# Kernel tuning notes

Measured on AMD Instinct MI355X. Metric: run time of the kernel, lower is better.

The kernel has to match this reference:

```python
import jax, jax.numpy as jnp
import numpy as np


def _diffuse(x, A):
    # x: [B,C,N,L], A: [B,V,W] -> out[b,c,v,l] = sum_w x[b,c,w,l] * A[b,v,w]
    return jnp.einsum('ncwl,nvw->ncvl', x, A)


def setup_inputs() -> dict:
    key = jax.random.key(0)
    kx, k0, k1, k2, kw = jax.random.split(key, 5)
    B, C, N, L = 32, 40, 512, 12
    C_OUT = 20
    C_CAT = 7 * C  # (order*support_len + 1) * c_in = (2*3+1)*40
    x = jax.random.normal(kx, (B, C, N, L), dtype=jnp.float32)
    def mk_support(k):
        a = jax.random.uniform(k, (B, N, N), dtype=jnp.float32)
        return a / jnp.sum(a, axis=-1, keepdims=True)  # row-normalized transition
    A0, A1, A2 = mk_support(k0), mk_support(k1), mk_support(k2)
    # Conv2d(c_cat, c_out, kernel=(1,2), dilation=2) weights, stored [c_out, c_cat, 2]
    W = jax.random.normal(kw, (C_OUT, C_CAT, 2), dtype=jnp.float32) * 0.05
    b = jnp.zeros((C_OUT,), dtype=jnp.float32)
    return {'x': x, 'A0': A0, 'A1': A1, 'A2': A2, 'W': W, 'b': b}


def reference(x, A0, A1, A2, W, b):
    # dgcn.forward (eval mode, dropout is identity): order=2, support_len=3
    out = [x]
    for A in (A0, A1, A2):
        x1 = _diffuse(x, A)
        out.append(x1)
        x2 = _diffuse(x1, A)
        out.append(x2)
    h = jnp.concatenate(out, axis=1)  # [B, 7C, N, L]
    # linear_: Conv2d kernel (1,2), dilation 2, no padding -> taps at t and t+2, L_out = L-2
    y = (jnp.einsum('ncvl,oc->novl', h[..., :-2], W[:, :, 0])
         + jnp.einsum('ncvl,oc->novl', h[..., 2:], W[:, :, 1])
         + b[None, :, None, None])
    return y
```

## Files before the change

kernel.cpp:

```cpp
#include <hip/hip_runtime.h>
#include <hip/hip_bf16.h>


typedef unsigned short u16;
typedef u16 u16x4 __attribute__((ext_vector_type(4)));
typedef u16 u16x8 __attribute__((ext_vector_type(8)));
typedef __bf16 bf16x8 __attribute__((ext_vector_type(8)));
typedef float f32x4 __attribute__((ext_vector_type(4)));

#define GLD_LDS16(g, l)  __builtin_amdgcn_global_load_lds( \
    (const __attribute__((address_space(1))) void*)(g),    \
    (__attribute__((address_space(3))) void*)(l), 16, 0, 0)

__device__ __forceinline__ u16 f2bf(float f) {
    unsigned int u = __float_as_uint(f);
    u += 0x7fffu + ((u >> 16) & 1u);
    return (u16)(u >> 16);
}
__device__ __forceinline__ float bf2f(u16 h) {
    return __uint_as_float(((unsigned int)h) << 16);
}

__global__ __launch_bounds__(256) void xpose(const float* __restrict__ x,
                                             u16* __restrict__ xq)
{
    const int t = threadIdx.x, vloc = t & 63, cg = t >> 6;
    const int v = blockIdx.x * 64 + vloc, b = blockIdx.y;

    u16 vals[12][12];
    #pragma unroll
    for (int ci = 0; ci < 12; ++ci) {
        int c = cg * 12 + ci;
        if (c < 40) {
            const float* xp = x + ((size_t)(b * 40 + c) * 512 + v) * 12;
            float4 f0 = *(const float4*)xp;
            float4 f1 = *(const float4*)(xp + 4);
            float4 f2 = *(const float4*)(xp + 8);
            vals[0][ci] = f2bf(f0.x);  vals[1][ci] = f2bf(f0.y);
            vals[2][ci] = f2bf(f0.z);  vals[3][ci] = f2bf(f0.w);
            vals[4][ci] = f2bf(f1.x);  vals[5][ci] = f2bf(f1.y);
            vals[6][ci] = f2bf(f1.z);  vals[7][ci] = f2bf(f1.w);
            vals[8][ci] = f2bf(f2.x);  vals[9][ci] = f2bf(f2.y);
            vals[10][ci] = f2bf(f2.z); vals[11][ci] = f2bf(f2.w);
        } else {
            #pragma unroll
            for (int l = 0; l < 12; ++l) vals[l][ci] = 0;
        }
    }
    #pragma unroll
    for (int l = 0; l < 12; ++l) {
        u16* dst = xq + ((size_t)(b * 12 + l) * 512 + v) * 48 + cg * 12;
        u16x4 a = { vals[l][0], vals[l][1], vals[l][2], vals[l][3] };
        u16x4 c4 = { vals[l][4], vals[l][5], vals[l][6], vals[l][7] };
        u16x4 d = { vals[l][8], vals[l][9], vals[l][10], vals[l][11] };
        *(u16x4*)(dst) = a;
        *(u16x4*)(dst + 4) = c4;
        *(u16x4*)(dst + 8) = d;
    }
}

__global__ __launch_bounds__(256) void proj_x(
    const u16* __restrict__ xq, const float* __restrict__ W,
    u16* __restrict__ P1, u16* __restrict__ P2, float* __restrict__ proj0)
{
    __shared__ u16 sA[144 * 104];
    __shared__ u16 sB[2][2 * 64 * 48];

    const int t = threadIdx.x, lane = t & 63, wid = t >> 6;
    const int b = blockIdx.y, v0 = blockIdx.x * 64;

    for (int id = t; id < 144 * 5; id += 256) {
        int m = id / 5, c0 = (id % 5) * 8;
        u16x8 e = {}, o8 = {};
        if (m < 140) {
            int o = m % 20, sg = m / 20;
            const float* wp = W + o * 560 + sg * 80 + c0 * 2;
            float4 a = *(const float4*)wp;
            float4 bb = *(const float4*)(wp + 4);
            float4 c = *(const float4*)(wp + 8);
            float4 d = *(const float4*)(wp + 12);
            e[0] = f2bf(a.x);  o8[0] = f2bf(a.y);  e[1] = f2bf(a.z);  o8[1] = f2bf(a.w);
            e[2] = f2bf(bb.x); o8[2] = f2bf(bb.y); e[3] = f2bf(bb.z); o8[3] = f2bf(bb.w);
            e[4] = f2bf(c.x);  o8[4] = f2bf(c.y);  e[5] = f2bf(c.z);  o8[5] = f2bf(c.w);
            e[6] = f2bf(d.x);  o8[6] = f2bf(d.y);  e[7] = f2bf(d.z);  o8[7] = f2bf(d.w);
        }
        *(u16x8*)(&sA[m * 104 + c0]) = e;
        *(u16x8*)(&sA[m * 104 + 40 + c0]) = o8;
    }
    for (int id = t; id < 144 * 3; id += 256) {
        int m = id / 3, k0 = 80 + (id % 3) * 8;
        u16x8 z = {};
        *(u16x8*)(&sA[m * 104 + k0]) = z;
    }

    auto stage = [&](int l, int buf) {
        u16* dst = &sB[buf][0];
        #pragma unroll
        for (int i = 0; i < 3; ++i) {
            int op = wid * 3 + i;
            int tap = op / 6, rem = op % 6;
            const u16* src = xq + ((size_t)(b * 12 + l + 2 * tap) * 512 + v0) * 48
                             + rem * 512 + lane * 8;
            GLD_LDS16(src, dst + tap * 3072 + rem * 512);
        }
    };

    stage(0, 0);
    __syncthreads();

    const int lr = lane & 15, q = lane >> 4;
    bf16x8 af[9][3];
    #pragma unroll
    for (int mf = 0; mf < 9; ++mf)
        #pragma unroll
        for (int s = 0; s < 3; ++s)
            af[mf][s] = *(const bf16x8*)(&sA[(mf * 16 + lr) * 104 + s * 32 + q * 8]);

    const int voff = (wid * 16 + lr) * 48;
    int boff[3];
    #pragma unroll
    for (int s = 0; s < 3; ++s) {
        int k = s * 32 + q * 8;
        int tap, c;
        if (k < 40)      { tap = 0; c = k; }
        else if (k < 80) { tap = 1; c = k - 40; }
        else             { tap = 1; c = 40; }
        boff[s] = tap * 3072 + voff + c;
    }

    const int v = v0 + wid * 16 + lr;
    for (int l = 0; l < 10; ++l) {
        const int cur = l & 1;
        if (l < 9) stage(l + 1, cur ^ 1);

        const u16* bb = &sB[cur][0];
        bf16x8 xf[3];
        #pragma unroll
        for (int s = 0; s < 3; ++s) xf[s] = *(const bf16x8*)(bb + boff[s]);

        f32x4 acc[9] = {};
        #pragma unroll
        for (int s = 0; s < 3; ++s)
            #pragma unroll
            for (int mf = 0; mf < 9; ++mf)
                acc[mf] = __builtin_amdgcn_mfma_f32_16x16x32_bf16(
                    af[mf][s], xf[s], acc[mf], 0, 0, 0);

        #pragma unroll
        for (int mf = 0; mf < 9; ++mf)
            #pragma unroll
            for (int i = 0; i < 4; ++i) {
                int m = mf * 16 + q * 4 + i;
                if (m < 140) {
                    int o = m % 20, sg = m / 20;
                    float val = acc[mf][i];
                    if (sg == 0) {
                        proj0[((size_t)(b * 20 + o) * 10 + l) * 512 + v] = val;
                    } else {
                        int s2 = (sg - 1) >> 1;
                        u16* dst = ((sg - 1) & 1) ? P2 : P1;
                        dst[((size_t)(s2 * 32 + b) * 200 + o * 10 + l) * 512 + v] = f2bf(val);
                    }
                }
            }
        __syncthreads();
    }
}

template <int EPI>
__device__ __forceinline__ void gemm_body(
    const float* __restrict__ A0, const float* __restrict__ A1, const float* __restrict__ A2,
    const u16* __restrict__ Xsrc, u16* __restrict__ Tdst, float* __restrict__ Ydst)
{
    __shared__ float sAf[2][128 * 32];
    __shared__ u16   sXs[2][112 * 32];

    const int bid = blockIdx.x;
    const int eid = (bid & 7) * 96 + (bid >> 3);
    const int z = eid >> 3, rem = eid & 7;
    const int vblk = (rem >> 1) * 128;
    const int colbase = (rem & 1) * 112;
    const int s = z >> 5, b = z & 31;

    const float* Af = (s == 0 ? A0 : (s == 1 ? A1 : A2)) + (size_t)b * 512 * 512;
    const u16* Xb = Xsrc + (size_t)z * 200 * 512;

    const int t = threadIdx.x;
    const int lane = t & 63, wid = t >> 6;
    const int lr = lane & 15;
    const int kc0 = (lane >> 4) * 2;

    auto stage = [&](int kt, int buf) {
        const int w0 = kt * 32;
        float* ab = &sAf[buf][0];
        u16*   xb = &sXs[buf][0];
        #pragma unroll
        for (int i = 0; i < 4; ++i) {
            int op  = wid * 4 + i;
            int row = op * 8 + (lane >> 3);
            int pc  = lane & 7;
            const float* src = Af + (size_t)(vblk + row) * 512 + w0 + ((pc ^ (row & 7)) << 2);
            GLD_LDS16(src, ab + op * 256);
        }
        #pragma unroll
        for (int i = 0; i < 2; ++i) {
            int op = wid + i * 4;
            if (op < 7) {
                int row = op * 16 + (lane >> 2);
                int ch  = lane & 3;
                const u16* src = Xb + (size_t)(colbase + row) * 512 + w0 + ch * 8;
                GLD_LDS16(src, xb + op * 512);
            }
        }
    };

    f32x4 acc[7][2] = {};

    stage(0, 0);
    __syncthreads();

    for (int kt = 0; kt < 16; ++kt) {
        const int cur = kt & 1;
        if (kt < 15) stage(kt + 1, cur ^ 1);

        bf16x8 af[2];
        #pragma unroll
        for (int mf = 0; mf < 2; ++mf) {
            int r = wid * 32 + mf * 16 + lr;
            const float* rb = &sAf[cur][r * 32];
            f32x4 a0 = *(const f32x4*)(rb + ((kc0 ^ (r & 7)) << 2));
            f32x4 a1 = *(const f32x4*)(rb + (((kc0 + 1) ^ (r & 7)) << 2));
            union { u16x8 u; bf16x8 bv; } cv;
            cv.u = (u16x8){ f2bf(a0[0]), f2bf(a0[1]), f2bf(a0[2]), f2bf(a0[3]),
                            f2bf(a1[0]), f2bf(a1[1]), f2bf(a1[2]), f2bf(a1[3]) };
            af[mf] = cv.bv;
        }
        #pragma unroll
        for (int cf = 0; cf < 7; ++cf) {
            bf16x8 xf = *(const bf16x8*)(&sXs[cur][(cf * 16 + lr) * 32 + (lane >> 4) * 8]);
            #pragma unroll
            for (int mf = 0; mf < 2; ++mf)
                acc[cf][mf] = __builtin_amdgcn_mfma_f32_16x16x32_bf16(
                    xf, af[mf], acc[cf][mf], 0, 0, 0);
        }
        __syncthreads();
    }

    const int r4 = (lane >> 4) * 4;
    if (EPI == 0) {
        u16* Tz = Tdst + (size_t)z * 200 * 512;
        #pragma unroll
        for (int cf = 0; cf < 7; ++cf)
            #pragma unroll
            for (int mf = 0; mf < 2; ++mf)
                #pragma unroll
                for (int i = 0; i < 4; ++i) {
                    int col = colbase + cf * 16 + r4 + i;
                    if (col < 200) {
                        size_t idx = (size_t)col * 512 + vblk + wid * 32 + mf * 16 + lr;
                        Tz[idx] = f2bf(acc[cf][mf][i] + bf2f(Tz[idx]));
                    }
                }
    } else {
        float* Yz = Ydst + (size_t)z * 200 * 512;
        #pragma unroll
        for (int cf = 0; cf < 7; ++cf)
            #pragma unroll
            for (int mf = 0; mf < 2; ++mf)
                #pragma unroll
                for (int i = 0; i < 4; ++i) {
                    int col = colbase + cf * 16 + r4 + i;
                    if (col < 200)
                        Yz[(size_t)col * 512 + vblk + wid * 32 + mf * 16 + lr] = acc[cf][mf][i];
                }
    }
}

__global__ __launch_bounds__(256) void gemm_t(
    const float* __restrict__ A0, const float* __restrict__ A1, const float* __restrict__ A2,
    const u16* __restrict__ P2, u16* __restrict__ T)
{
    gemm_body<0>(A0, A1, A2, P2, T, nullptr);
}

__global__ __launch_bounds__(256) void gemm_yp(
    const float* __restrict__ A0, const float* __restrict__ A1, const float* __restrict__ A2,
    const u16* __restrict__ T, float* __restrict__ Ypart)
{
    gemm_body<1>(A0, A1, A2, T, nullptr, Ypart);
}

__global__ __launch_bounds__(256) void reduce_y(
    const float* __restrict__ Ypart, const float* __restrict__ proj0,
    const float* __restrict__ bias, float* __restrict__ y)
{
    int i = blockIdx.x * 256 + threadIdx.x;
    if (i >= 32 * 20 * 512) return;
    int v = i & 511;
    int r = i >> 9;
    int o = r % 20, b = r / 20;
    float bb = bias[o];
    float* yp = y + ((size_t)r * 512 + v) * 10;
    #pragma unroll
    for (int l = 0; l < 10; ++l) {
        float sum = proj0[((size_t)r * 10 + l) * 512 + v] + bb;
        #pragma unroll
        for (int s = 0; s < 3; ++s)
            sum += Ypart[((size_t)(s * 32 + b) * 200 + o * 10 + l) * 512 + v];
        yp[l] = sum;
    }
}

extern "C" void kernel_launch(void* const* d_in, const int* in_sizes, int n_in,
                              void* d_out, int out_size, void* d_ws, size_t ws_size,
                              hipStream_t stream) {
    const float* x    = (const float*)d_in[0];
    const float* A0   = (const float*)d_in[1];
    const float* A1   = (const float*)d_in[2];
    const float* A2   = (const float*)d_in[3];
    const float* W    = (const float*)d_in[4];
    const float* bias = (const float*)d_in[5];
    float* y = (float*)d_out;

    const size_t PSZ = (size_t)96 * 200 * 512;
    u16* P1 = (u16*)d_ws;
    u16* P2 = P1 + PSZ;
    float* proj0 = (float*)(P2 + PSZ);
    float* Ypart = proj0 + (size_t)32 * 20 * 10 * 512;
    u16* xq = (u16*)Ypart;

    xpose<<<dim3(8, 32), 256, 0, stream>>>(x, xq);
    proj_x<<<dim3(8, 32), 256, 0, stream>>>(xq, W, P1, P2, proj0);
    gemm_t<<<dim3(768), 256, 0, stream>>>(A0, A1, A2, P2, P1);
    gemm_yp<<<dim3(768), 256, 0, stream>>>(A0, A1, A2, P1, Ypart);
    reduce_y<<<dim3(1280), 256, 0, stream>>>(Ypart, proj0, bias, y);
}
```

Measured before the change: 105.2 us.

## Pre-convert supports to bf16, triple-buffer GEMMs, fuse support reduction into second GEMM

Adds a pass that converts the three fp32 support matrices to bf16 once, so both GEMMs load half the bytes and skip per-tile conversion. The GEMMs become a three-stage pipeline using explicit vmcnt waits and swizzled bf16 LDS tiles. The second GEMM now loops over all three supports in its K dimension and writes the final output with proj0 and bias, which removes the Ypart buffer and the reduce kernel. The cost is an extra conversion kernel that reads and writes about 100MB, plus fewer blocks (512) for the second GEMM, each with a longer K loop.

```diff
diff --git a/kernel.cpp b/kernel.cpp
--- a/kernel.cpp
+++ b/kernel.cpp
@@ -167,148 +167,207 @@
     }
 }
 
-template <int EPI>
-__device__ __forceinline__ void gemm_body(
-    const float* __restrict__ A0, const float* __restrict__ A1, const float* __restrict__ A2,
-    const u16* __restrict__ Xsrc, u16* __restrict__ Tdst, float* __restrict__ Ydst)
-{
-    __shared__ float sAf[2][128 * 32];
-    __shared__ u16   sXs[2][112 * 32];
+__global__ __launch_bounds__(256) void a2bf(
+    const float* __restrict__ A0, const float* __restrict__ A1,
+    const float* __restrict__ A2, u16* __restrict__ Abf)
+{
+    const int s = blockIdx.y;
+    const float* src = (s == 0 ? A0 : (s == 1 ? A1 : A2));
+    size_t i = ((size_t)blockIdx.x * 256 + threadIdx.x) * 8;
+    float4 f0 = *(const float4*)(src + i);
+    float4 f1 = *(const float4*)(src + i + 4);
+    u16x8 o = { f2bf(f0.x), f2bf(f0.y), f2bf(f0.z), f2bf(f0.w),
+                f2bf(f1.x), f2bf(f1.y), f2bf(f1.z), f2bf(f1.w) };
+    *(u16x8*)(Abf + (size_t)s * 8388608 + i) = o;
+}
+
+__global__ __launch_bounds__(256) void gemm_t(
+    const u16* __restrict__ Abf, const u16* __restrict__ P2, u16* __restrict__ T)
+{
+    __shared__ u16 sA[3 * 4096];
+    __shared__ u16 sX[3 * 4096];
 
     const int bid = blockIdx.x;
     const int eid = (bid & 7) * 96 + (bid >> 3);
     const int z = eid >> 3, rem = eid & 7;
     const int vblk = (rem >> 1) * 128;
-    const int colbase = (rem & 1) * 112;
-    const int s = z >> 5, b = z & 31;
-
-    const float* Af = (s == 0 ? A0 : (s == 1 ? A1 : A2)) + (size_t)b * 512 * 512;
-    const u16* Xb = Xsrc + (size_t)z * 200 * 512;
+    const int colbase = (rem & 1) * 128;
+
+    const u16* Az = Abf + (size_t)z * 262144;
+    const u16* Xb = P2 + (size_t)z * 102400;
 
     const int t = threadIdx.x;
     const int lane = t & 63, wid = t >> 6;
-    const int lr = lane & 15;
-    const int kc0 = (lane >> 4) * 2;
+    const int lr = lane & 15, q = lane >> 4;
+    const int rsub = lane >> 2, csub = lane & 3;
 
     auto stage = [&](int kt, int buf) {
         const int w0 = kt * 32;
-        float* ab = &sAf[buf][0];
-        u16*   xb = &sXs[buf][0];
-        #pragma unroll
-        for (int i = 0; i < 4; ++i) {
-            int op  = wid * 4 + i;
-            int row = op * 8 + (lane >> 3);
-            int pc  = lane & 7;
-            const float* src = Af + (size_t)(vblk + row) * 512 + w0 + ((pc ^ (row & 7)) << 2);
-            GLD_LDS16(src, ab + op * 256);
-        }
+        u16* ab = &sA[buf * 4096];
+        u16* xb = &sX[buf * 4096];
         #pragma unroll
         for (int i = 0; i < 2; ++i) {
-            int op = wid + i * 4;
-            if (op < 7) {
-                int row = op * 16 + (lane >> 2);
-                int ch  = lane & 3;
-                const u16* src = Xb + (size_t)(colbase + row) * 512 + w0 + ch * 8;
-                GLD_LDS16(src, xb + op * 512);
-            }
+            int op = wid * 2 + i;
+            int r = op * 16 + rsub;
+            const u16* src = Az + (size_t)(vblk + r) * 512 + w0 + ((csub ^ ((r >> 1) & 3)) * 8);
+            GLD_LDS16(src, ab + op * 512);
+        }
+        #pragma unroll
+        for (int i = 0; i < 2; ++i) {
+            int op = wid * 2 + i;
+            int r = op * 16 + rsub;
+            const u16* src = Xb + (size_t)(colbase + r) * 512 + w0 + ((csub ^ ((r >> 1) & 3)) * 8);
+            GLD_LDS16(src, xb + op * 512);
         }
     };
 
-    f32x4 acc[7][2] = {};
-
-    stage(0, 0);
-    __syncthreads();
-
+    f32x4 acc[8][2] = {};
+    stage(0, 0); stage(1, 1); stage(2, 2);
+
+    int cur = 0;
     for (int kt = 0; kt < 16; ++kt) {
-        const int cur = kt & 1;
-        if (kt < 15) stage(kt + 1, cur ^ 1);
-
+        if (kt < 14)       { asm volatile("s_waitcnt vmcnt(8)" ::: "memory"); }
+        else if (kt == 14) { asm volatile("s_waitcnt vmcnt(4)" ::: "memory"); }
+        else               { asm volatile("s_waitcnt vmcnt(0)" ::: "memory"); }
+        __builtin_amdgcn_s_barrier();
+        __builtin_amdgcn_sched_barrier(0);
+
+        const u16* ab = &sA[cur * 4096];
+        const u16* xb = &sX[cur * 4096];
         bf16x8 af[2];
         #pragma unroll
         for (int mf = 0; mf < 2; ++mf) {
             int r = wid * 32 + mf * 16 + lr;
-            const float* rb = &sAf[cur][r * 32];
-            f32x4 a0 = *(const f32x4*)(rb + ((kc0 ^ (r & 7)) << 2));
-            f32x4 a1 = *(const f32x4*)(rb + (((kc0 + 1) ^ (r & 7)) << 2));
-            union { u16x8 u; bf16x8 bv; } cv;
-            cv.u = (u16x8){ f2bf(a0[0]), f2bf(a0[1]), f2bf(a0[2]), f2bf(a0[3]),
-                            f2bf(a1[0]), f2bf(a1[1]), f2bf(a1[2]), f2bf(a1[3]) };
-            af[mf] = cv.bv;
-        }
-        #pragma unroll
-        for (int cf = 0; cf < 7; ++cf) {
-            bf16x8 xf = *(const bf16x8*)(&sXs[cur][(cf * 16 + lr) * 32 + (lane >> 4) * 8]);
+            af[mf] = *(const bf16x8*)(ab + r * 32 + ((q ^ ((r >> 1) & 3)) * 8));
+        }
+        #pragma unroll
+        for (int cf = 0; cf < 8; ++cf) {
+            int rx = cf * 16 + lr;
+            bf16x8 xf = *(const bf16x8*)(xb + rx * 32 + ((q ^ ((rx >> 1) & 3)) * 8));
             #pragma unroll
             for (int mf = 0; mf < 2; ++mf)
                 acc[cf][mf] = __builtin_amdgcn_mfma_f32_16x16x32_bf16(
                     xf, af[mf], acc[cf][mf], 0, 0, 0);
         }
-        __syncthreads();
-    }
-
-    const int r4 = (lane >> 4) * 4;
-    if (EPI == 0) {
-        u16* Tz = Tdst + (size_t)z * 200 * 512;
-        #pragma unroll
-        for (int cf = 0; cf < 7; ++cf)
+
+        if (kt < 13) {
+            asm volatile("s_waitcnt lgkmcnt(0)" ::: "memory");
+            __builtin_amdgcn_s_barrier();
+            __builtin_amdgcn_sched_barrier(0);
+            stage(kt + 3, cur);
+        }
+        cur = (cur == 2) ? 0 : cur + 1;
+    }
+
+    u16* Tz = T + (size_t)z * 102400;
+    #pragma unroll
+    for (int cf = 0; cf < 8; ++cf)
+        #pragma unroll
+        for (int mf = 0; mf < 2; ++mf)
+            #pragma unroll
+            for (int i = 0; i < 4; ++i) {
+                int col = colbase + cf * 16 + q * 4 + i;
+                if (col < 200) {
+                    size_t idx = (size_t)col * 512 + vblk + wid * 32 + mf * 16 + lr;
+                    Tz[idx] = f2bf(acc[cf][mf][i] + bf2f(Tz[idx]));
+                }
+            }
+}
+
+__global__ __launch_bounds__(256) void gemm_yp(
+    const u16* __restrict__ Abf, const u16* __restrict__ T,
+    const float* __restrict__ proj0, const float* __restrict__ bias,
+    float* __restrict__ y)
+{
+    __shared__ u16 sA[3 * 2048];
+    __shared__ u16 sX[3 * 4096];
+
+    const int bid = blockIdx.x;
+    const int eid = (bid & 7) * 64 + (bid >> 3);
+    const int b = eid >> 4, rem = eid & 15;
+    const int vblk = (rem >> 1) * 64;
+    const int colbase = (rem & 1) * 128;
+
+    const int t = threadIdx.x;
+    const int lane = t & 63, wid = t >> 6;
+    const int lr = lane & 15, q = lane >> 4;
+    const int rsub = lane >> 2, csub = lane & 3;
+    const int wv = wid & 1, wc = wid >> 1;
+
+    auto stage = [&](int kt, int buf) {
+        const int s = kt >> 4, w0 = (kt & 15) * 32;
+        const u16* Az = Abf + (size_t)(s * 32 + b) * 262144;
+        const u16* Xz = T + (size_t)(s * 32 + b) * 102400;
+        u16* ab = &sA[buf * 2048];
+        u16* xb = &sX[buf * 4096];
+        {
+            int r = wid * 16 + rsub;
+            const u16* src = Az + (size_t)(vblk + r) * 512 + w0 + ((csub ^ ((r >> 1) & 3)) * 8);
+            GLD_LDS16(src, ab + wid * 512);
+        }
+        #pragma unroll
+        for (int i = 0; i < 2; ++i) {
+            int op = wid * 2 + i;
+            int r = op * 16 + rsub;
+            const u16* src = Xz + (size_t)(colbase + r) * 512 + w0 + ((csub ^ ((r >> 1) & 3)) * 8);
+            GLD_LDS16(src, xb + op * 512);
+        }
+    };
+
+    f32x4 acc[4][2] = {};
+    stage(0, 0); stage(1, 1); stage(2, 2);
+
+    int cur = 0;
+    for (int kt = 0; kt < 48; ++kt) {
+        if (kt < 46)       { asm volatile("s_waitcnt vmcnt(6)" ::: "memory"); }
+        else if (kt == 46) { asm volatile("s_waitcnt vmcnt(3)" ::: "memory"); }
+        else               { asm volatile("s_waitcnt vmcnt(0)" ::: "memory"); }
+        __builtin_amdgcn_s_barrier();
+        __builtin_amdgcn_sched_barrier(0);
+
+        const u16* ab = &sA[cur * 2048];
+        const u16* xb = &sX[cur * 4096];
+        bf16x8 af[2];
+        #pragma unroll
+        for (int mf = 0; mf < 2; ++mf) {
+            int r = wv * 32 + mf * 16 + lr;
+            af[mf] = *(const bf16x8*)(ab + r * 32 + ((q ^ ((r >> 1) & 3)) * 8));
+        }
+        #pragma unroll
+        for (int cf = 0; cf < 4; ++cf) {
+            int rx = wc * 64 + cf * 16 + lr;
+            bf16x8 xf = *(const bf16x8*)(xb + rx * 32 + ((q ^ ((rx >> 1) & 3)) * 8));
             #pragma unroll
             for (int mf = 0; mf < 2; ++mf)
-                #pragma unroll
-                for (int i = 0; i < 4; ++i) {
-                    int col = colbase + cf * 16 + r4 + i;
-                    if (col < 200) {
-                        size_t idx = (size_t)col * 512 + vblk + wid * 32 + mf * 16 + lr;
-                        Tz[idx] = f2bf(acc[cf][mf][i] + bf2f(Tz[idx]));
-                    }
+                acc[cf][mf] = __builtin_amdgcn_mfma_f32_16x16x32_bf16(
+                    xf, af[mf], acc[cf][mf], 0, 0, 0);
+        }
+
+        if (kt < 45) {
+            asm volatile("s_waitcnt lgkmcnt(0)" ::: "memory");
+            __builtin_amdgcn_s_barrier();
+            __builtin_amdgcn_sched_barrier(0);
+            stage(kt + 3, cur);
+        }
+        cur = (cur == 2) ? 0 : cur + 1;
+    }
+
+    #pragma unroll
+    for (int cf = 0; cf < 4; ++cf)
+        #pragma unroll
+        for (int mf = 0; mf < 2; ++mf)
+            #pragma unroll
+            for (int i = 0; i < 4; ++i) {
+                int col = colbase + wc * 64 + cf * 16 + q * 4 + i;
+                if (col < 200) {
+                    int o = col / 10, l = col - o * 10;
+                    int v = vblk + wv * 32 + mf * 16 + lr;
+                    float val = acc[cf][mf][i]
+                              + proj0[((size_t)(b * 20 + o) * 10 + l) * 512 + v]
+                              + bias[o];
+                    y[((size_t)(b * 20 + o) * 512 + v) * 10 + l] = val;
                 }
-    } else {
-        float* Yz = Ydst + (size_t)z * 200 * 512;
-        #pragma unroll
-        for (int cf = 0; cf < 7; ++cf)
-            #pragma unroll
-            for (int mf = 0; mf < 2; ++mf)
-                #pragma unroll
-                for (int i = 0; i < 4; ++i) {
-                    int col = colbase + cf * 16 + r4 + i;
-                    if (col < 200)
-                        Yz[(size_t)col * 512 + vblk + wid * 32 + mf * 16 + lr] = acc[cf][mf][i];
-                }
-    }
-}
-
-__global__ __launch_bounds__(256) void gemm_t(
-    const float* __restrict__ A0, const float* __restrict__ A1, const float* __restrict__ A2,
-    const u16* __restrict__ P2, u16* __restrict__ T)
-{
-    gemm_body<0>(A0, A1, A2, P2, T, nullptr);
-}
-
-__global__ __launch_bounds__(256) void gemm_yp(
-    const float* __restrict__ A0, const float* __restrict__ A1, const float* __restrict__ A2,
-    const u16* __restrict__ T, float* __restrict__ Ypart)
-{
-    gemm_body<1>(A0, A1, A2, T, nullptr, Ypart);
-}
-
-__global__ __launch_bounds__(256) void reduce_y(
-    const float* __restrict__ Ypart, const float* __restrict__ proj0,
-    const float* __restrict__ bias, float* __restrict__ y)
-{
-    int i = blockIdx.x * 256 + threadIdx.x;
-    if (i >= 32 * 20 * 512) return;
-    int v = i & 511;
-    int r = i >> 9;
-    int o = r % 20, b = r / 20;
-    float bb = bias[o];
-    float* yp = y + ((size_t)r * 512 + v) * 10;
-    #pragma unroll
-    for (int l = 0; l < 10; ++l) {
-        float sum = proj0[((size_t)r * 10 + l) * 512 + v] + bb;
-        #pragma unroll
-        for (int s = 0; s < 3; ++s)
-            sum += Ypart[((size_t)(s * 32 + b) * 200 + o * 10 + l) * 512 + v];
-        yp[l] = sum;
-    }
+            }
 }
 
 extern "C" void kernel_launch(void* const* d_in, const int* in_sizes, int n_in,
@@ -326,12 +385,13 @@
     u16* P1 = (u16*)d_ws;
     u16* P2 = P1 + PSZ;
     float* proj0 = (float*)(P2 + PSZ);
-    float* Ypart = proj0 + (size_t)32 * 20 * 10 * 512;
-    u16* xq = (u16*)Ypart;
+    u16* shared_region = (u16*)(proj0 + (size_t)32 * 20 * 10 * 512);
+    u16* xq  = shared_region;
+    u16* Abf = shared_region;
 
     xpose<<<dim3(8, 32), 256, 0, stream>>>(x, xq);
     proj_x<<<dim3(8, 32), 256, 0, stream>>>(xq, W, P1, P2, proj0);
-    gemm_t<<<dim3(768), 256, 0, stream>>>(A0, A1, A2, P2, P1);
-    gemm_yp<<<dim3(768), 256, 0, stream>>>(A0, A1, A2, P1, Ypart);
-    reduce_y<<<dim3(1280), 256, 0, stream>>>(Ypart, proj0, bias, y);
-}
+    a2bf<<<dim3(4096, 3), 256, 0, stream>>>(A0, A1, A2, Abf);
+    gemm_t<<<dim3(768), 256, 0, stream>>>(Abf, P2, P1);
+    gemm_yp<<<dim3(512), 256, 0, stream>>>(Abf, P1, proj0, bias, y);
+}
```

After: 148.6 us. 1.41x slower.
